# Performance work log

Measured on AMD Instinct MI355X. Metric: run time of the kernel, lower is better.

## Reference

```python
import jax, jax.numpy as jnp
import numpy as np

N, E, D, R, G, C = 100000, 600000, 128, 4, 256, 16
EPS = 1e-5

def _rgcn(x, src, dst, edge_type, w_rel, w_root, b):
    # out_i = x_i @ W_root + b + sum_r mean_{j in N_r(i)} x_j @ W_r  (PyG RGCNConv, aggr='mean')
    x_src = x[src]                                   # [E, D] gather
    out = x @ w_root + b                             # [N, D]
    for r in range(R):
        m = (edge_type == r).astype(x.dtype)         # [E]
        msg = (x_src @ w_rel[r]) * m[:, None]        # [E, D]
        agg = jax.ops.segment_sum(msg, dst, num_segments=N)
        cnt = jax.ops.segment_sum(m, dst, num_segments=N)
        out = out + agg / jnp.maximum(cnt, 1.0)[:, None]
    return out

def _bn_eval(x, gamma, beta, mean, var):
    return (x - mean) * jax.lax.rsqrt(var + EPS) * gamma + beta

def setup_inputs() -> dict:
    key = jax.random.key(0)
    ks = jax.random.split(key, 12)
    x = jax.random.normal(ks[0], (N, D), dtype=jnp.float32)
    edge_index = jax.random.randint(ks[1], (2, E), 0, N)
    edge_type = jax.random.randint(ks[2], (E,), 0, R)
    batch = jnp.sort(jax.random.randint(ks[3], (N,), 0, G))
    s = 1.0 / np.sqrt(D)
    conv_rel_w = jax.random.normal(ks[4], (3, R, D, D), dtype=jnp.float32) * s
    conv_root_w = jax.random.normal(ks[5], (3, D, D), dtype=jnp.float32) * s
    conv_bias = jnp.zeros((3, D), dtype=jnp.float32)
    bn_gamma = jnp.ones((2, D), dtype=jnp.float32)
    bn_beta = jnp.zeros((2, D), dtype=jnp.float32)
    bn_mean = jax.random.normal(ks[6], (2, D), dtype=jnp.float32) * 0.1
    bn_var = jax.random.uniform(ks[7], (2, D), minval=0.5, maxval=1.5, dtype=jnp.float32)
    cls_w1 = jax.random.normal(ks[8], (D, D // 2), dtype=jnp.float32) * s
    cls_b1 = jnp.zeros((D // 2,), dtype=jnp.float32)
    cls_w2 = jax.random.normal(ks[9], (D // 2, C), dtype=jnp.float32) / np.sqrt(D // 2)
    cls_b2 = jnp.zeros((C,), dtype=jnp.float32)
    return {"x": x, "edge_index": edge_index, "edge_type": edge_type, "batch": batch,
            "conv_rel_w": conv_rel_w, "conv_root_w": conv_root_w, "conv_bias": conv_bias,
            "bn_gamma": bn_gamma, "bn_beta": bn_beta, "bn_mean": bn_mean, "bn_var": bn_var,
            "cls_w1": cls_w1, "cls_b1": cls_b1, "cls_w2": cls_w2, "cls_b2": cls_b2}

def reference(x, edge_index, edge_type, batch, conv_rel_w, conv_root_w, conv_bias,
              bn_gamma, bn_beta, bn_mean, bn_var, cls_w1, cls_b1, cls_w2, cls_b2):
    src, dst = edge_index[0], edge_index[1]
    prev = None
    h = x
    for i in range(3):
        h_new = _rgcn(h, src, dst, edge_type, conv_rel_w[i], conv_root_w[i], conv_bias[i])
        if prev is not None:
            h_new = h_new + prev  # residual (shapes always match: D==D)
        if i != 2:
            h_new = _bn_eval(h_new, bn_gamma[i], bn_beta[i], bn_mean[i], bn_var[i])
            h_new = jax.nn.elu(h_new)  # alpha=1; dropout inactive in eval
        prev = h_new
        h = h_new
    # global mean pool over graphs
    sums = jax.ops.segment_sum(h, batch, num_segments=G)          # [G, D]
    cnts = jax.ops.segment_sum(jnp.ones((N,), h.dtype), batch, num_segments=G)
    pooled = sums / jnp.maximum(cnts, 1.0)[:, None]
    z = jax.nn.elu(pooled @ cls_w1 + cls_b1)
    logits = z @ cls_w2 + cls_b2
    return jax.nn.log_softmax(logits, axis=-1)
```

## Files before the change

### kernel.cpp

```cpp
#include <hip/hip_runtime.h>
#include <hip/hip_bf16.h>

#define NN 100000
#define EE 600000
#define DD 128
#define GG 256
#define CCL 16

typedef __attribute__((ext_vector_type(8))) short short8;
typedef __attribute__((ext_vector_type(4))) float f32x4;
typedef const __attribute__((address_space(1))) void* gas_t;
typedef __attribute__((address_space(3))) void* las_t;

__device__ __forceinline__ void async_ld16(const void* g, void* l) {
    __builtin_amdgcn_global_load_lds((gas_t)g, (las_t)l, 16, 0, 0);
}
__device__ __forceinline__ unsigned short f2bf(float x) {
    unsigned u = __float_as_uint(x);
    unsigned r = (u + 0x7FFFu + ((u >> 16) & 1u)) >> 16;
    return (unsigned short)r;
}
__device__ __forceinline__ float bf2f(unsigned short b) {
    return __uint_as_float(((unsigned)b) << 16);
}
__device__ __forceinline__ void unpack8(uint4 v, float* f) {
    f[0] = __uint_as_float(v.x << 16); f[1] = __uint_as_float(v.x & 0xFFFF0000u);
    f[2] = __uint_as_float(v.y << 16); f[3] = __uint_as_float(v.y & 0xFFFF0000u);
    f[4] = __uint_as_float(v.z << 16); f[5] = __uint_as_float(v.z & 0xFFFF0000u);
    f[6] = __uint_as_float(v.w << 16); f[7] = __uint_as_float(v.w & 0xFFFF0000u);
}

__global__ __launch_bounds__(256) void sniff_kernel(const void* __restrict__ xraw, int* __restrict__ flag) {
    int t = threadIdx.x;
    const unsigned short* u = (const unsigned short*)xraw;
    int good = 0;
    #pragma unroll
    for (int i = 0; i < 4; i++) {
        unsigned short b = u[t * 4 + i];
        int e = (b >> 7) & 0xFF;
        if (e >= 107 && e <= 130) good++;
    }
    __shared__ int sg[256];
    sg[t] = good;
    __syncthreads();
    for (int s = 128; s > 0; s >>= 1) { if (t < s) sg[t] += sg[t + s]; __syncthreads(); }
    if (t == 0) flag[0] = (sg[0] >= 900) ? 1 : 0;
}

__device__ __forceinline__ float loadf(const void* p, size_t i, int isbf) {
    if (isbf) return bf2f(((const unsigned short*)p)[i]);
    return ((const float*)p)[i];
}

__global__ __launch_bounds__(256) void convx_kernel(const void* __restrict__ xraw, const int* __restrict__ flag,
                                                    __hip_bfloat16* __restrict__ xc) {
    int isbf = flag[0];
    size_t i0 = ((size_t)blockIdx.x * 256 + threadIdx.x) * 8;
    if (i0 >= (size_t)NN * DD) return;
    if (isbf) {
        *(uint4*)(xc + i0) = *(const uint4*)((const __hip_bfloat16*)xraw + i0);
    } else {
        const float* xf = (const float*)xraw;
        unsigned short o[8];
        #pragma unroll
        for (int j = 0; j < 8; j++) o[j] = f2bf(xf[i0 + j]);
        *(uint4*)(xc + i0) = *(uint4*)o;
    }
}

__global__ __launch_bounds__(256) void convw_kernel(const void* __restrict__ rel_raw, const void* __restrict__ root_raw,
                                                    const int* __restrict__ flag, __hip_bfloat16* __restrict__ wt) {
    int isbf = flag[0];
    int mat = blockIdx.x;
    int layer = mat / 5, g = mat % 5;
    size_t srcoff = (g == 0) ? (size_t)layer * 16384 : (size_t)(layer * 4 + (g - 1)) * 16384;
    const void* sraw = (g == 0) ? root_raw : rel_raw;
    __hip_bfloat16* dstp = wt + (size_t)layer * 81920 + g * 128;
    for (int idx = threadIdx.x; idx < 16384; idx += 256) {
        int kk = idx >> 7, n = idx & 127;
        float v = loadf(sraw, srcoff + (size_t)kk * 128 + n, isbf);
        dstp[(size_t)n * 640 + kk] = __float2bfloat16(v);
    }
}

__global__ __launch_bounds__(256) void convp_kernel(const void* bias, const void* bng, const void* bnb,
                                                    const void* bnm, const void* bnv, const void* w1,
                                                    const void* b1, const void* w2, const void* b2,
                                                    const int* __restrict__ flag, float* __restrict__ pf) {
    int isbf = flag[0];
    int b = blockIdx.x, t = threadIdx.x;
    if (b < 9) {
        const void* srcs[9] = {bias, bng, bnb, bnm, bnv, w1, b1, w2, b2};
        const int cnts[9] = {384, 256, 256, 256, 256, 8192, 64, 1024, 16};
        const int offs[9] = {0, 384, 640, 896, 1152, 1408, 9600, 9664, 10688};
        const void* s = srcs[b];
        int c = cnts[b], o = offs[b];
        for (int i = t; i < c; i += 256) pf[o + i] = loadf(s, i, isbf);
    } else {
        int bl = b - 9;
        if (t < 128) {
            float iva = rsqrtf(loadf(bnv, bl * 128 + t, isbf) + 1e-5f);
            float gm = loadf(bng, bl * 128 + t, isbf) * iva;
            float ga = loadf(bnb, bl * 128 + t, isbf) - loadf(bnm, bl * 128 + t, isbf) * gm;
            pf[11008 + bl * 256 + t] = gm;
            pf[11008 + bl * 256 + 128 + t] = ga;
        }
    }
}

__global__ __launch_bounds__(256) void count4_kernel(const int* __restrict__ dst, const int* __restrict__ et,
                                                     int* __restrict__ cnt4) {
    int e = blockIdx.x * 256 + threadIdx.x;
    if (e < EE) atomicAdd(&cnt4[dst[e] * 4 + et[e]], 1);
}

__global__ __launch_bounds__(256) void allocn_kernel(const int* __restrict__ cnt4, int* __restrict__ counter,
                                                     int* __restrict__ startn, int* __restrict__ wptr4) {
    int n = blockIdx.x * 256 + threadIdx.x;
    int lane = threadIdx.x & 63;
    int4 cv = make_int4(0, 0, 0, 0);
    int c = 0;
    if (n < NN) {
        cv = *(const int4*)(cnt4 + n * 4);
        c = cv.x + cv.y + cv.z + cv.w;
    }
    int v = c;
    #pragma unroll
    for (int d = 1; d < 64; d <<= 1) {
        int o = __shfl_up(v, d);
        if (lane >= d) v += o;
    }
    int base = 0;
    if (lane == 63) base = atomicAdd(counter, v);
    base = __shfl(base, 63);
    if (n < NN) {
        int s = base + v - c;
        startn[n] = s;
        wptr4[n * 4 + 0] = s;
        wptr4[n * 4 + 1] = s + cv.x;
        wptr4[n * 4 + 2] = s + cv.x + cv.y;
        wptr4[n * 4 + 3] = s + cv.x + cv.y + cv.z;
    }
}

__global__ __launch_bounds__(256) void fill4_kernel(const int* __restrict__ src, const int* __restrict__ dst,
                                                    const int* __restrict__ et, int* __restrict__ wptr4,
                                                    int* __restrict__ esrc) {
    int e = blockIdx.x * 256 + threadIdx.x;
    if (e < EE) {
        int pos = atomicAdd(&wptr4[dst[e] * 4 + et[e]], 1);
        esrc[pos] = src[e];
    }
}

__global__ __launch_bounds__(256) void agg_kernel(const __hip_bfloat16* __restrict__ h,
                                                  const int* __restrict__ esrc,
                                                  const int* __restrict__ startn,
                                                  const int* __restrict__ cnt4,
                                                  __hip_bfloat16* __restrict__ Abuf) {
    int node = blockIdx.x * 16 + (threadIdx.x >> 4);
    int c16 = threadIdx.x & 15;
    int col0 = c16 * 8;
    int4 cv = *(const int4*)(cnt4 + node * 4);
    int s = startn[node];
    int cr[4] = {cv.x, cv.y, cv.z, cv.w};
    #pragma unroll
    for (int r = 0; r < 4; r++) {
        int c = cr[r];
        float a[8];
        #pragma unroll
        for (int j = 0; j < 8; j++) a[j] = 0.f;
        int i = 0;
        for (; i + 4 <= c; i += 4) {
            int s4[4];
            uint4 vv[4];
            #pragma unroll
            for (int q = 0; q < 4; q++) s4[q] = esrc[s + i + q];
            #pragma unroll
            for (int q = 0; q < 4; q++) vv[q] = *(const uint4*)(h + (size_t)s4[q] * 128 + col0);
            #pragma unroll
            for (int q = 0; q < 4; q++) {
                float f[8];
                unpack8(vv[q], f);
                #pragma unroll
                for (int j = 0; j < 8; j++) a[j] += f[j];
            }
        }
        for (; i < c; i++) {
            int sq = esrc[s + i];
            uint4 v0 = *(const uint4*)(h + (size_t)sq * 128 + col0);
            float f[8];
            unpack8(v0, f);
            #pragma unroll
            for (int j = 0; j < 8; j++) a[j] += f[j];
        }
        float w = (c > 0) ? (1.f / (float)c) : 0.f;
        unsigned short u[8];
        #pragma unroll
        for (int j = 0; j < 8; j++) u[j] = f2bf(a[j] * w);
        *(uint4*)(Abuf + (size_t)node * 512 + r * 128 + col0) = *(uint4*)u;
        s += c;
    }
}

__global__ __launch_bounds__(512) void rgemm_kernel(const __hip_bfloat16* __restrict__ h_in,
                                                    const __hip_bfloat16* __restrict__ Abuf,
                                                    const __hip_bfloat16* __restrict__ wtL,
                                                    const float* __restrict__ bias,
                                                    const float* __restrict__ gmp,
                                                    const float* __restrict__ gap,
                                                    const __hip_bfloat16* __restrict__ hres,
                                                    __hip_bfloat16* __restrict__ hout,
                                                    int do_bn) {
    __shared__ __align__(16) short ldsb[40960];
    int t = threadIdx.x;
    int wv = t >> 6, lane = t & 63, quad = lane >> 4, r16 = lane & 15;
    int m0 = blockIdx.x * 128;
    int nh = blockIdx.y;

    #pragma unroll
    for (int i = 0; i < 10; i++) {
        int u = i * 512 + t;
        int nl = u / 80;
        int segp = u - nl * 80;
        int seg = segp ^ (nl & 7);
        async_ld16(wtL + (size_t)(nh * 64 + nl) * 640 + seg * 8, &ldsb[u * 8]);
    }

    int r0 = m0 + wv * 16 + r16;       if (r0 > NN - 1) r0 = NN - 1;

    short8 a[20];
    #pragma unroll
    for (int j = 0; j < 4; j++)  a[j] = *(const short8*)(h_in + (size_t)r0 * 128 + j * 32 + quad * 8);
    #pragma unroll
    for (int j = 4; j < 10; j++) a[j] = *(const short8*)(Abuf + (size_t)r0 * 512 + (j - 4) * 32 + quad * 8);
    __syncthreads();

    #pragma unroll
    for (int j = 10; j < 20; j++) a[j] = *(const short8*)(Abuf + (size_t)r0 * 512 + (j - 4) * 32 + quad * 8);

    f32x4 acc[4];
    #pragma unroll
    for (int nt = 0; nt < 4; nt++) acc[nt] = (f32x4){0.f, 0.f, 0.f, 0.f};

    #pragma unroll
    for (int j = 0; j < 20; j++) {
        #pragma unroll
        for (int nt = 0; nt < 4; nt++) {
            int nl = nt * 16 + r16;
            int unit = nl * 80 + ((j * 4 + quad) ^ (nl & 7));
            short8 b = *(const short8*)&ldsb[unit * 8];
            acc[nt] = __builtin_amdgcn_mfma_f32_16x16x32_bf16(a[j], b, acc[nt], 0, 0, 0);
        }
    }

    __syncthreads();
    float* cf = (float*)ldsb;
    #pragma unroll
    for (int nt = 0; nt < 4; nt++) {
        int col = nt * 16 + r16;
        #pragma unroll
        for (int reg = 0; reg < 4; reg++) {
            cf[(wv * 16 + quad * 4 + reg) * 66 + col] = acc[nt][reg];
        }
    }
    __syncthreads();
    #pragma unroll
    for (int it = 0; it < 2; it++) {
        int u4 = it * 512 + t;
        int row = u4 >> 3, oct = u4 & 7;
        int onode = m0 + row;
        if (onode < NN) {
            int gc = nh * 64 + oct * 8;
            const float* cp = cf + row * 66 + oct * 8;
            float a8[8];
            #pragma unroll
            for (int j = 0; j < 8; j++) a8[j] = cp[j] + bias[gc + j];
            if (hres) {
                float rf[8];
                unpack8(*(const uint4*)(hres + (size_t)onode * 128 + gc), rf);
                #pragma unroll
                for (int j = 0; j < 8; j++) a8[j] += rf[j];
            }
            if (do_bn) {
                #pragma unroll
                for (int j = 0; j < 8; j++) {
                    float z = a8[j] * gmp[gc + j] + gap[gc + j];
                    a8[j] = z > 0.f ? z : expm1f(z);
                }
            }
            unsigned short u[8];
            #pragma unroll
            for (int j = 0; j < 8; j++) u[j] = f2bf(a8[j]);
            *(uint4*)(hout + (size_t)onode * 128 + gc) = *(uint4*)u;
        }
    }
}

__global__ __launch_bounds__(256) void pool_kernel(const __hip_bfloat16* __restrict__ h3,
                                                   const int* __restrict__ batch,
                                                   float* __restrict__ pooled) {
    int g = blockIdx.x, t = threadIdx.x;
    int rowpar = t >> 4, colg = t & 15;
    int lo = 0, hi = NN;
    while (lo < hi) { int mid = (lo + hi) >> 1; if (batch[mid] < g) lo = mid + 1; else hi = mid; }
    int s0 = lo;
    hi = NN;
    while (lo < hi) { int mid = (lo + hi) >> 1; if (batch[mid] < g + 1) lo = mid + 1; else hi = mid; }
    int s1 = lo;
    float a[8];
    #pragma unroll
    for (int j = 0; j < 8; j++) a[j] = 0.f;
    for (int n = s0 + rowpar; n < s1; n += 16) {
        float f[8];
        unpack8(*(const uint4*)(h3 + (size_t)n * 128 + colg * 8), f);
        #pragma unroll
        for (int j = 0; j < 8; j++) a[j] += f[j];
    }
    __shared__ float sd[16][128];
    #pragma unroll
    for (int j = 0; j < 8; j++) sd[rowpar][colg * 8 + j] = a[j];
    __syncthreads();
    if (t < 128) {
        float sum = 0.f;
        #pragma unroll
        for (int i = 0; i < 16; i++) sum += sd[i][t];
        int cgn = s1 - s0;
        pooled[g * 128 + t] = sum / (float)(cgn > 0 ? cgn : 1);
    }
}

__global__ __launch_bounds__(64) void cls_kernel(const float* __restrict__ pooled,
                                                 const float* __restrict__ pf,
                                                 const int* __restrict__ flag,
                                                 void* __restrict__ out) {
    int g = blockIdx.x, j = threadIdx.x;
    const float* w1 = pf + 1408;
    const float* b1 = pf + 9600;
    const float* w2 = pf + 9664;
    const float* b2 = pf + 10688;
    __shared__ float z[64];
    __shared__ float lg[16];
    const float* p = pooled + g * 128;
    float acc = b1[j];
    for (int d = 0; d < 128; d++) acc += p[d] * w1[d * 64 + j];
    acc = acc > 0.f ? acc : expm1f(acc);
    z[j] = acc;
    __syncthreads();
    if (j < CCL) {
        float l = b2[j];
        for (int k = 0; k < 64; k++) l += z[k] * w2[k * 16 + j];
        lg[j] = l;
    }
    __syncthreads();
    if (j < CCL) {
        float m = lg[0];
        for (int k = 1; k < CCL; k++) m = fmaxf(m, lg[k]);
        float s = 0.f;
        for (int k = 0; k < CCL; k++) s += expf(lg[k] - m);
        float val = lg[j] - m - logf(s);
        if (flag[0]) ((__hip_bfloat16*)out)[g * CCL + j] = __float2bfloat16(val);
        else         ((float*)out)[g * CCL + j] = val;
    }
}

extern "C" void kernel_launch(void* const* d_in, const int* in_sizes, int n_in,
                              void* d_out, int out_size, void* d_ws, size_t ws_size,
                              hipStream_t stream) {
    const void* x_raw    = d_in[0];
    const int* ei        = (const int*)d_in[1];
    const int* et        = (const int*)d_in[2];
    const int* batch     = (const int*)d_in[3];
    const void* rel_raw  = d_in[4];
    const void* root_raw = d_in[5];
    const int* srcp = ei;
    const int* dstp = ei + EE;

    char* ws = (char*)d_ws;
    size_t off = 0;
    auto take = [&](size_t bytes) { size_t r = off; off += (bytes + 1023) & ~(size_t)1023; return r; };
    __hip_bfloat16* Abuf  = (__hip_bfloat16*)(ws + take((size_t)NN * 512 * 2));
    __hip_bfloat16* xc    = (__hip_bfloat16*)(ws + take((size_t)NN * 128 * 2));
    __hip_bfloat16* hA    = (__hip_bfloat16*)(ws + take((size_t)NN * 128 * 2));
    __hip_bfloat16* hB    = (__hip_bfloat16*)(ws + take((size_t)NN * 128 * 2));
    __hip_bfloat16* hC    = (__hip_bfloat16*)(ws + take((size_t)NN * 128 * 2));
    __hip_bfloat16* wt    = (__hip_bfloat16*)(ws + take((size_t)3 * 81920 * 2));
    float* pf             = (float*)(ws + take((size_t)11520 * 4));
    float* pooled         = (float*)(ws + take((size_t)GG * 128 * 4));
    int* cnt4             = (int*)(ws + take((size_t)NN * 16 + 8));
    int* counter          = cnt4 + NN * 4;
    int* flag             = cnt4 + NN * 4 + 1;
    int* startn           = (int*)(ws + take((size_t)NN * 4));
    int* wptr4            = (int*)(ws + take((size_t)NN * 16));
    int* esrc             = (int*)(ws + take((size_t)EE * 4));

    hipMemsetAsync(cnt4, 0, (size_t)NN * 16 + 4, stream);
    sniff_kernel<<<1, 256, 0, stream>>>(x_raw, flag);
    convx_kernel<<<(NN * DD / 8 + 255) / 256, 256, 0, stream>>>(x_raw, flag, xc);
    convw_kernel<<<15, 256, 0, stream>>>(rel_raw, root_raw, flag, wt);
    convp_kernel<<<11, 256, 0, stream>>>(d_in[6], d_in[7], d_in[8], d_in[9], d_in[10],
                                         d_in[11], d_in[12], d_in[13], d_in[14], flag, pf);
    count4_kernel<<<(EE + 255) / 256, 256, 0, stream>>>(dstp, et, cnt4);
    allocn_kernel<<<(NN + 255) / 256, 256, 0, stream>>>(cnt4, counter, startn, wptr4);
    fill4_kernel<<<(EE + 255) / 256, 256, 0, stream>>>(srcp, dstp, et, wptr4, esrc);

    const __hip_bfloat16* hin = xc;
    __hip_bfloat16* houts[3] = {hA, hB, hC};
    for (int l = 0; l < 3; l++) {
        int bl = l < 2 ? l : 1;
        agg_kernel<<<NN / 16, 256, 0, stream>>>(hin, esrc, startn, cnt4, Abuf);
        rgemm_kernel<<<dim3((NN + 127) / 128, 2), 512, 0, stream>>>(
            hin, Abuf, wt + (size_t)l * 81920, pf + l * 128,
            pf + 11008 + bl * 256, pf + 11008 + bl * 256 + 128,
            (l > 0) ? hin : (const __hip_bfloat16*)nullptr, houts[l], (l < 2) ? 1 : 0);
        hin = houts[l];
    }
    pool_kernel<<<GG, 256, 0, stream>>>(houts[2], batch, pooled);
    cls_kernel<<<GG, 64, 0, stream>>>(pooled, pf, flag, (void*)d_out);
}
```

Baseline: 597.7 us.

## Fuse neighbor aggregation into the relational GEMM kernel, dropping the Abuf round trip

The separate per-node mean-aggregation kernel is merged into the GEMM kernel. Each lane gathers and averages neighbor rows straight into the MFMA A-fragment registers, so the 100MB Abuf is never written to or read back from global memory. The kernel now computes both output halves in one block, reloading the second half of the weights into LDS between them. The cost is fewer, larger blocks (782 instead of 1564) with heavy register use from the 20 A fragments plus 32 accumulators. The gather loop is also more serialized, which may lower occupancy and latency hiding for the random neighbor gathers.

```diff
diff --git a/kernel.cpp b/kernel.cpp
--- a/kernel.cpp
+++ b/kernel.cpp
@@ -153,146 +153,158 @@
     }
 }
 
-__global__ __launch_bounds__(256) void agg_kernel(const __hip_bfloat16* __restrict__ h,
-                                                  const int* __restrict__ esrc,
-                                                  const int* __restrict__ startn,
-                                                  const int* __restrict__ cnt4,
-                                                  __hip_bfloat16* __restrict__ Abuf) {
-    int node = blockIdx.x * 16 + (threadIdx.x >> 4);
-    int c16 = threadIdx.x & 15;
-    int col0 = c16 * 8;
-    int4 cv = *(const int4*)(cnt4 + node * 4);
-    int s = startn[node];
-    int cr[4] = {cv.x, cv.y, cv.z, cv.w};
-    #pragma unroll
-    for (int r = 0; r < 4; r++) {
-        int c = cr[r];
-        float a[8];
-        #pragma unroll
-        for (int j = 0; j < 8; j++) a[j] = 0.f;
-        int i = 0;
-        for (; i + 4 <= c; i += 4) {
-            int s4[4];
-            uint4 vv[4];
-            #pragma unroll
-            for (int q = 0; q < 4; q++) s4[q] = esrc[s + i + q];
-            #pragma unroll
-            for (int q = 0; q < 4; q++) vv[q] = *(const uint4*)(h + (size_t)s4[q] * 128 + col0);
-            #pragma unroll
-            for (int q = 0; q < 4; q++) {
-                float f[8];
-                unpack8(vv[q], f);
-                #pragma unroll
-                for (int j = 0; j < 8; j++) a[j] += f[j];
-            }
-        }
-        for (; i < c; i++) {
-            int sq = esrc[s + i];
-            uint4 v0 = *(const uint4*)(h + (size_t)sq * 128 + col0);
-            float f[8];
-            unpack8(v0, f);
-            #pragma unroll
-            for (int j = 0; j < 8; j++) a[j] += f[j];
-        }
-        float w = (c > 0) ? (1.f / (float)c) : 0.f;
-        unsigned short u[8];
-        #pragma unroll
-        for (int j = 0; j < 8; j++) u[j] = f2bf(a[j] * w);
-        *(uint4*)(Abuf + (size_t)node * 512 + r * 128 + col0) = *(uint4*)u;
-        s += c;
-    }
-}
-
-__global__ __launch_bounds__(512) void rgemm_kernel(const __hip_bfloat16* __restrict__ h_in,
-                                                    const __hip_bfloat16* __restrict__ Abuf,
-                                                    const __hip_bfloat16* __restrict__ wtL,
-                                                    const float* __restrict__ bias,
-                                                    const float* __restrict__ gmp,
-                                                    const float* __restrict__ gap,
-                                                    const __hip_bfloat16* __restrict__ hres,
-                                                    __hip_bfloat16* __restrict__ hout,
-                                                    int do_bn) {
+__global__ __launch_bounds__(512) void flayer_kernel(const __hip_bfloat16* __restrict__ h_in,
+                                                     const int* __restrict__ esrc,
+                                                     const int* __restrict__ startn,
+                                                     const int* __restrict__ cnt4,
+                                                     const __hip_bfloat16* __restrict__ wtL,
+                                                     const float* __restrict__ bias,
+                                                     const float* __restrict__ gmp,
+                                                     const float* __restrict__ gap,
+                                                     const __hip_bfloat16* __restrict__ hres,
+                                                     __hip_bfloat16* __restrict__ hout,
+                                                     int do_bn) {
     __shared__ __align__(16) short ldsb[40960];
+    __shared__ __align__(16) float cf[128 * 66];
     int t = threadIdx.x;
     int wv = t >> 6, lane = t & 63, quad = lane >> 4, r16 = lane & 15;
     int m0 = blockIdx.x * 128;
-    int nh = blockIdx.y;
+    int node = m0 + wv * 16 + r16;
+    if (node > NN - 1) node = NN - 1;
 
     #pragma unroll
     for (int i = 0; i < 10; i++) {
         int u = i * 512 + t;
         int nl = u / 80;
-        int segp = u - nl * 80;
-        int seg = segp ^ (nl & 7);
-        async_ld16(wtL + (size_t)(nh * 64 + nl) * 640 + seg * 8, &ldsb[u * 8]);
-    }
-
-    int r0 = m0 + wv * 16 + r16;       if (r0 > NN - 1) r0 = NN - 1;
-
-    short8 a[20];
-    #pragma unroll
-    for (int j = 0; j < 4; j++)  a[j] = *(const short8*)(h_in + (size_t)r0 * 128 + j * 32 + quad * 8);
-    #pragma unroll
-    for (int j = 4; j < 10; j++) a[j] = *(const short8*)(Abuf + (size_t)r0 * 512 + (j - 4) * 32 + quad * 8);
-    __syncthreads();
-
-    #pragma unroll
-    for (int j = 10; j < 20; j++) a[j] = *(const short8*)(Abuf + (size_t)r0 * 512 + (j - 4) * 32 + quad * 8);
+        int seg = (u - nl * 80) ^ (nl & 7);
+        async_ld16(wtL + (size_t)nl * 640 + seg * 8, &ldsb[u * 8]);
+    }
+
+    short8 A[20];
+    {
+        const __hip_bfloat16* hp = h_in + (size_t)node * 128 + quad * 8;
+        #pragma unroll
+        for (int kc = 0; kc < 4; kc++) A[kc] = *(const short8*)(hp + kc * 32);
+    }
+    int s = startn[node];
+    int4 cvv = *(const int4*)(cnt4 + node * 4);
+    int cr[4] = {cvv.x, cvv.y, cvv.z, cvv.w};
+    #pragma unroll
+    for (int r = 0; r < 4; r++) {
+        int c = cr[r];
+        float g[4][8];
+        #pragma unroll
+        for (int kc = 0; kc < 4; kc++)
+            #pragma unroll
+            for (int j = 0; j < 8; j++) g[kc][j] = 0.f;
+        int i = 0;
+        for (; i + 2 <= c; i += 2) {
+            int e0 = esrc[s + i];
+            int e1 = esrc[s + i + 1];
+            const __hip_bfloat16* p0 = h_in + (size_t)e0 * 128 + quad * 8;
+            const __hip_bfloat16* p1 = h_in + (size_t)e1 * 128 + quad * 8;
+            uint4 v0[4], v1[4];
+            #pragma unroll
+            for (int kc = 0; kc < 4; kc++) v0[kc] = *(const uint4*)(p0 + kc * 32);
+            #pragma unroll
+            for (int kc = 0; kc < 4; kc++) v1[kc] = *(const uint4*)(p1 + kc * 32);
+            #pragma unroll
+            for (int kc = 0; kc < 4; kc++) {
+                float f[8];
+                unpack8(v0[kc], f);
+                #pragma unroll
+                for (int j = 0; j < 8; j++) g[kc][j] += f[j];
+                unpack8(v1[kc], f);
+                #pragma unroll
+                for (int j = 0; j < 8; j++) g[kc][j] += f[j];
+            }
+        }
+        if (i < c) {
+            int e0 = esrc[s + i];
+            const __hip_bfloat16* p0 = h_in + (size_t)e0 * 128 + quad * 8;
+            #pragma unroll
+            for (int kc = 0; kc < 4; kc++) {
+                uint4 v = *(const uint4*)(p0 + kc * 32);
+                float f[8];
+                unpack8(v, f);
+                #pragma unroll
+                for (int j = 0; j < 8; j++) g[kc][j] += f[j];
+            }
+        }
+        float w = (c > 0) ? (1.f / (float)c) : 0.f;
+        #pragma unroll
+        for (int kc = 0; kc < 4; kc++) {
+            short8 tmp;
+            #pragma unroll
+            for (int j = 0; j < 8; j++) tmp[j] = (short)f2bf(g[kc][j] * w);
+            A[4 + r * 4 + kc] = tmp;
+        }
+        s += c;
+    }
 
     f32x4 acc[4];
     #pragma unroll
-    for (int nt = 0; nt < 4; nt++) acc[nt] = (f32x4){0.f, 0.f, 0.f, 0.f};
-
-    #pragma unroll
-    for (int j = 0; j < 20; j++) {
+    for (int half = 0; half < 2; half++) {
+        __syncthreads();
+        #pragma unroll
+        for (int nt = 0; nt < 4; nt++) acc[nt] = (f32x4){0.f, 0.f, 0.f, 0.f};
+        #pragma unroll
+        for (int j = 0; j < 20; j++) {
+            #pragma unroll
+            for (int nt = 0; nt < 4; nt++) {
+                int nl = nt * 16 + r16;
+                int unit = nl * 80 + ((j * 4 + quad) ^ (nl & 7));
+                short8 b = *(const short8*)&ldsb[unit * 8];
+                acc[nt] = __builtin_amdgcn_mfma_f32_16x16x32_bf16(A[j], b, acc[nt], 0, 0, 0);
+            }
+        }
+        __syncthreads();
+        if (half == 0) {
+            #pragma unroll
+            for (int i = 0; i < 10; i++) {
+                int u = i * 512 + t;
+                int nl = u / 80;
+                int seg = (u - nl * 80) ^ (nl & 7);
+                async_ld16(wtL + (size_t)(64 + nl) * 640 + seg * 8, &ldsb[u * 8]);
+            }
+        }
         #pragma unroll
         for (int nt = 0; nt < 4; nt++) {
-            int nl = nt * 16 + r16;
-            int unit = nl * 80 + ((j * 4 + quad) ^ (nl & 7));
-            short8 b = *(const short8*)&ldsb[unit * 8];
-            acc[nt] = __builtin_amdgcn_mfma_f32_16x16x32_bf16(a[j], b, acc[nt], 0, 0, 0);
-        }
-    }
-
-    __syncthreads();
-    float* cf = (float*)ldsb;
-    #pragma unroll
-    for (int nt = 0; nt < 4; nt++) {
-        int col = nt * 16 + r16;
-        #pragma unroll
-        for (int reg = 0; reg < 4; reg++) {
-            cf[(wv * 16 + quad * 4 + reg) * 66 + col] = acc[nt][reg];
-        }
-    }
-    __syncthreads();
-    #pragma unroll
-    for (int it = 0; it < 2; it++) {
-        int u4 = it * 512 + t;
-        int row = u4 >> 3, oct = u4 & 7;
-        int onode = m0 + row;
-        if (onode < NN) {
-            int gc = nh * 64 + oct * 8;
-            const float* cp = cf + row * 66 + oct * 8;
-            float a8[8];
-            #pragma unroll
-            for (int j = 0; j < 8; j++) a8[j] = cp[j] + bias[gc + j];
-            if (hres) {
-                float rf[8];
-                unpack8(*(const uint4*)(hres + (size_t)onode * 128 + gc), rf);
+            int col = nt * 16 + r16;
+            #pragma unroll
+            for (int reg = 0; reg < 4; reg++)
+                cf[(wv * 16 + quad * 4 + reg) * 66 + col] = acc[nt][reg];
+        }
+        __syncthreads();
+        #pragma unroll
+        for (int it = 0; it < 2; it++) {
+            int u4 = it * 512 + t;
+            int row = u4 >> 3, oct = u4 & 7;
+            int onode = m0 + row;
+            if (onode < NN) {
+                int gc = half * 64 + oct * 8;
+                const float* cp = cf + row * 66 + oct * 8;
+                float a8[8];
                 #pragma unroll
-                for (int j = 0; j < 8; j++) a8[j] += rf[j];
+                for (int j = 0; j < 8; j++) a8[j] = cp[j] + bias[gc + j];
+                if (hres) {
+                    float rf[8];
+                    unpack8(*(const uint4*)(hres + (size_t)onode * 128 + gc), rf);
+                    #pragma unroll
+                    for (int j = 0; j < 8; j++) a8[j] += rf[j];
+                }
+                if (do_bn) {
+                    #pragma unroll
+                    for (int j = 0; j < 8; j++) {
+                        float z = a8[j] * gmp[gc + j] + gap[gc + j];
+                        a8[j] = z > 0.f ? z : expm1f(z);
+                    }
+                }
+                unsigned short u[8];
+                #pragma unroll
+                for (int j = 0; j < 8; j++) u[j] = f2bf(a8[j]);
+                *(uint4*)(hout + (size_t)onode * 128 + gc) = *(uint4*)u;
             }
-            if (do_bn) {
-                #pragma unroll
-                for (int j = 0; j < 8; j++) {
-                    float z = a8[j] * gmp[gc + j] + gap[gc + j];
-                    a8[j] = z > 0.f ? z : expm1f(z);
-                }
-            }
-            unsigned short u[8];
-            #pragma unroll
-            for (int j = 0; j < 8; j++) u[j] = f2bf(a8[j]);
-            *(uint4*)(hout + (size_t)onode * 128 + gc) = *(uint4*)u;
         }
     }
 }
@@ -379,7 +391,6 @@
     char* ws = (char*)d_ws;
     size_t off = 0;
     auto take = [&](size_t bytes) { size_t r = off; off += (bytes + 1023) & ~(size_t)1023; return r; };
-    __hip_bfloat16* Abuf  = (__hip_bfloat16*)(ws + take((size_t)NN * 512 * 2));
     __hip_bfloat16* xc    = (__hip_bfloat16*)(ws + take((size_t)NN * 128 * 2));
     __hip_bfloat16* hA    = (__hip_bfloat16*)(ws + take((size_t)NN * 128 * 2));
     __hip_bfloat16* hB    = (__hip_bfloat16*)(ws + take((size_t)NN * 128 * 2));
@@ -408,9 +419,8 @@
     __hip_bfloat16* houts[3] = {hA, hB, hC};
     for (int l = 0; l < 3; l++) {
         int bl = l < 2 ? l : 1;
-        agg_kernel<<<NN / 16, 256, 0, stream>>>(hin, esrc, startn, cnt4, Abuf);
-        rgemm_kernel<<<dim3((NN + 127) / 128, 2), 512, 0, stream>>>(
-            hin, Abuf, wt + (size_t)l * 81920, pf + l * 128,
+        flayer_kernel<<<(NN + 127) / 128, 512, 0, stream>>>(
+            hin, esrc, startn, cnt4, wt + (size_t)l * 81920, pf + l * 128,
             pf + 11008 + bl * 256, pf + 11008 + bl * 256 + 128,
             (l > 0) ? hin : (const __hip_bfloat16*)nullptr, houts[l], (l < 2) ? 1 : 0);
         hin = houts[l];
```

Result: no change. 607.3 us (+1.6%).
